# Kernel optimization log

Hardware: AMD Instinct MI355X
Metric: run time of the kernel (lower is better)

The kernel has to match this reference:

```python
import jax, jax.numpy as jnp
import numpy as np

N_USERS = 100000
N_ITEMS = 50000
N_EDGES = 1600000
EMBED = 128
LAYER = 128


def setup_inputs() -> dict:
    key = jax.random.key(0)
    k1, k2, k3, k4, k5 = jax.random.split(key, 5)
    item_emb = jax.random.normal(k1, (N_ITEMS, EMBED), dtype=jnp.float32)
    # per-user mean normalization (1/degree); use uniform positive values
    user_n_j = jax.random.uniform(k2, (N_USERS, 1), dtype=jnp.float32)
    mean_weight = jax.random.normal(k3, (EMBED, LAYER), dtype=jnp.float32) * (1.0 / np.sqrt(EMBED))
    adj_vals = jnp.ones((N_EDGES,), dtype=jnp.float32)
    adj_rows = jax.random.randint(k4, (N_EDGES,), 0, N_USERS, dtype=jnp.int32)
    adj_cols = jax.random.randint(k5, (N_EDGES,), 0, N_ITEMS, dtype=jnp.int32)
    return {
        "item_emb": item_emb,
        "user_n_j": user_n_j,
        "mean_weight": mean_weight,
        "adj_vals": adj_vals,
        "adj_rows": adj_rows,
        "adj_cols": adj_cols,
        "n_users": N_USERS,
    }


def reference(item_emb, user_n_j, mean_weight, adj_vals, adj_rows, adj_cols, n_users):
    # e_k = sparse.mm(adj, item_emb): gather item rows per edge, scale by edge
    # value, scatter-add into destination user rows.
    edge_feat = adj_vals[:, None] * item_emb[adj_cols]          # [E, D]
    e_k = jax.ops.segment_sum(edge_feat, adj_rows, num_segments=n_users)  # [U, D]
    e_k = e_k * user_n_j                                        # neighbor-mean scale
    return e_k @ mean_weight                                    # [U, layer]
```

## Files before the change

### kernel.cpp

```cpp
#include <hip/hip_runtime.h>
#include <hip/hip_bf16.h>

#define D 128
#define BSHIFT 6
#define BUSERS (1 << BSHIFT)
#define NBLK 256
#define CHUNK 1280
#define MROWS 64

typedef __attribute__((ext_vector_type(8))) short bf16x8;
typedef __attribute__((ext_vector_type(4))) float f32x4;

__device__ __forceinline__ unsigned int bf16rn(float f) {
  unsigned int u = __float_as_uint(f);
  return (u + 0x7fffu + ((u >> 16) & 1u)) >> 16;
}

__device__ __forceinline__ void pw_tile(
    const float* __restrict__ emb, const float* __restrict__ W,
    unsigned short* __restrict__ Pb, int n_items, int tile,
    unsigned short* Wt ) {
  const int tid = threadIdx.x;
  const int m0 = tile * MROWS;

  for (int i = tid; i < 128 * 128; i += 256) {
    const int k = i >> 7, c = i & 127;
    const unsigned short v = (unsigned short)bf16rn(W[i]);
    const int boff = c * 256 + ((2 * k) ^ ((c & 7) << 4));
    *reinterpret_cast<unsigned short*>(reinterpret_cast<char*>(Wt) + boff) = v;
  }

  const int w = tid >> 6;
  const int lane = tid & 63;
  const int lr = lane & 15;
  const int lg = lane >> 4;

  bf16x8 a[4];
  const int gr = m0 + w * 16 + lr;
#pragma unroll
  for (int ks = 0; ks < 4; ++ks) {
    float4 f0 = {0.f, 0.f, 0.f, 0.f}, f1 = {0.f, 0.f, 0.f, 0.f};
    if (gr < n_items) {
      const float* p = emb + (size_t)gr * 128 + ks * 32 + lg * 8;
      f0 = *reinterpret_cast<const float4*>(p);
      f1 = *reinterpret_cast<const float4*>(p + 4);
    }
    bf16x8 av;
    av[0] = (short)bf16rn(f0.x); av[1] = (short)bf16rn(f0.y);
    av[2] = (short)bf16rn(f0.z); av[3] = (short)bf16rn(f0.w);
    av[4] = (short)bf16rn(f1.x); av[5] = (short)bf16rn(f1.y);
    av[6] = (short)bf16rn(f1.z); av[7] = (short)bf16rn(f1.w);
    a[ks] = av;
  }
  __syncthreads();

  f32x4 acc[8];
#pragma unroll
  for (int cs = 0; cs < 8; ++cs) acc[cs] = {0.f, 0.f, 0.f, 0.f};

#pragma unroll
  for (int cs = 0; cs < 8; ++cs) {
    const int c = cs * 16 + lr;
#pragma unroll
    for (int ks = 0; ks < 4; ++ks) {
      const int boff = c * 256 + (((ks * 64) + lg * 16) ^ ((lr & 7) << 4));
      const bf16x8 b = *reinterpret_cast<const bf16x8*>(
          reinterpret_cast<const char*>(Wt) + boff);
      acc[cs] = __builtin_amdgcn_mfma_f32_16x16x32_bf16(a[ks], b, acc[cs],
                                                        0, 0, 0);
    }
  }

#pragma unroll
  for (int cs = 0; cs < 8; ++cs) {
    const int c = cs * 16 + lr;
#pragma unroll
    for (int reg = 0; reg < 4; ++reg) {
      const int r = m0 + w * 16 + lg * 4 + reg;
      if (r < n_items)
        Pb[(size_t)r * 128 + c] = (unsigned short)bf16rn(acc[cs][reg]);
    }
  }
}

__global__ __launch_bounds__(256) void pw_hist_kernel(
    const float* __restrict__ emb, const float* __restrict__ W,
    unsigned short* __restrict__ Pb, int n_items, int npw1,
    const int* __restrict__ rows, int* __restrict__ bcount, int n_edges,
    int epb, int nbuck) {
  __shared__ __align__(16) char smem[32768];
  const int tid = threadIdx.x;

  if ((int)blockIdx.x < npw1) {
    pw_tile(emb, W, Pb, n_items, blockIdx.x, (unsigned short*)smem);
  } else {
    int* h = (int*)smem;
    const int hb = blockIdx.x - npw1;
    for (int b = tid; b < nbuck; b += 256) h[b] = 0;
    __syncthreads();
    const int e0 = hb * epb;
    const int e1 = (e0 + epb < n_edges) ? e0 + epb : n_edges;
    for (int e = e0 + tid; e < e1; e += 256)
      atomicAdd(&h[rows[e] >> BSHIFT], 1);
    __syncthreads();
    for (int b = tid; b < nbuck; b += 256)
      bcount[(size_t)b * NBLK + hb] = h[b];
  }
}

__global__ __launch_bounds__(1024) void blocksum_kernel(
    const int* __restrict__ in, int* __restrict__ partials, int n) {
  __shared__ int lds[1024];
  const int tid = threadIdx.x;
  const int i = blockIdx.x * 1024 + tid;
  lds[tid] = (i < n) ? in[i] : 0;
  __syncthreads();
  for (int s = 512; s > 0; s >>= 1) {
    if (tid < s) lds[tid] += lds[tid + s];
    __syncthreads();
  }
  if (tid == 0) partials[blockIdx.x] = lds[0];
}

__global__ __launch_bounds__(1024) void scanpart_kernel(
    const int* __restrict__ partials, int* __restrict__ blockoff, int nb) {
  __shared__ int lds[1024];
  const int tid = threadIdx.x;
  const int x = (tid < nb) ? partials[tid] : 0;
  lds[tid] = x;
  __syncthreads();
  for (int s = 1; s < 1024; s <<= 1) {
    const int y = (tid >= s) ? lds[tid - s] : 0;
    __syncthreads();
    lds[tid] += y;
    __syncthreads();
  }
  if (tid < nb) blockoff[tid] = lds[tid] - x;
}

__global__ __launch_bounds__(1024) void localscan_kernel(
    const int* __restrict__ in, const int* __restrict__ blockoff,
    int* __restrict__ base, int n) {
  __shared__ int lds[1024];
  const int tid = threadIdx.x;
  const int i = blockIdx.x * 1024 + tid;
  const int x = (i < n) ? in[i] : 0;
  lds[tid] = x;
  __syncthreads();
  for (int s = 1; s < 1024; s <<= 1) {
    const int y = (tid >= s) ? lds[tid - s] : 0;
    __syncthreads();
    lds[tid] += y;
    __syncthreads();
  }
  if (i < n) base[i] = blockoff[blockIdx.x] + lds[tid] - x;
}

__global__ __launch_bounds__(256) void scatter_pw_kernel(
    const int* __restrict__ rows, const int* __restrict__ cols,
    const float* __restrict__ vals, const int* __restrict__ base,
    int2* __restrict__ sedge, int n_edges, int epb, int nbuck,
    const float* __restrict__ emb, const float* __restrict__ W,
    unsigned short* __restrict__ Pb, int n_items, int npw1) {
  __shared__ __align__(16) char smem[32768];
  const int tid = threadIdx.x;

  if ((int)blockIdx.x >= NBLK) {
    pw_tile(emb, W, Pb, n_items, npw1 + (int)blockIdx.x - NBLK,
            (unsigned short*)smem);
    return;
  }
  int* cur = (int*)smem;
  for (int b = tid; b < nbuck; b += 256)
    cur[b] = base[(size_t)b * NBLK + blockIdx.x];
  __syncthreads();
  const int e0 = blockIdx.x * epb;
  const int e1 = (e0 + epb < n_edges) ? e0 + epb : n_edges;
  for (int e = e0 + tid; e < e1; e += 256) {
    const int r = rows[e];
    const int pos = atomicAdd(&cur[r >> BSHIFT], 1);
    sedge[pos] =
        make_int2(((r & (BUSERS - 1)) << 16) | cols[e], __float_as_int(vals[e]));
  }
}

__global__ __launch_bounds__(256) void bucket_gather_kernel(
    const uint4* __restrict__ Pb4,
    const int* __restrict__ base, const int2* __restrict__ sedge,
    const float* __restrict__ nj, float* __restrict__ out, int n_users,
    int n_edges, int nbuck) {
  __shared__ int2 eraw[CHUNK];
  __shared__ int2 esort[CHUNK];
  __shared__ int cnt[BUSERS];
  __shared__ int incl[BUSERS];

  const int tid = threadIdx.x;
  const int b = blockIdx.x;
  const int u0 = b << BSHIFT;
  const int qw = tid >> 4;
  const int l16 = tid & 15;

  const int beg = base[(size_t)b * NBLK];
  const int end = (b + 1 < nbuck) ? base[(size_t)(b + 1) * NBLK] : n_edges;

  float4 acc0[4], acc1[4];
#pragma unroll
  for (int k = 0; k < 4; ++k) {
    acc0[k] = {0.f, 0.f, 0.f, 0.f};
    acc1[k] = {0.f, 0.f, 0.f, 0.f};
  }

  for (int cbeg = beg; cbeg < end; cbeg += CHUNK) {
    const int cnum = (cbeg + CHUNK < end) ? CHUNK : (end - cbeg);
    if (tid < BUSERS) cnt[tid] = 0;
    __syncthreads();
    for (int i = tid; i < cnum; i += 256) {
      const int2 e = sedge[cbeg + i];
      eraw[i] = e;
      atomicAdd(&cnt[((unsigned int)e.x) >> 16], 1);
    }
    __syncthreads();
    if (tid < BUSERS) incl[tid] = cnt[tid];
    __syncthreads();
    for (int s = 1; s < BUSERS; s <<= 1) {
      int y = 0;
      if (tid < BUSERS && tid >= s) y = incl[tid - s];
      __syncthreads();
      if (tid < BUSERS) incl[tid] += y;
      __syncthreads();
    }
    if (tid < BUSERS) cnt[tid] = incl[tid] - cnt[tid];
    __syncthreads();
    for (int i = tid; i < cnum; i += 256) {
      const int2 e = eraw[i];
      const int pos = atomicAdd(&cnt[((unsigned int)e.x) >> 16], 1);
      esort[pos] = e;
    }
    __syncthreads();

    if (cnum > 0) {
#pragma unroll
      for (int k = 0; k < 4; ++k) {
        const int ul = qw * 4 + k;
        const int s = (ul == 0) ? 0 : incl[ul - 1];
        const int t = incl[ul];
        const int ub = ((qw >> 2) << 4) + k;
        int wlen = 0;
#pragma unroll
        for (int m = 0; m < 4; ++m) {
          const int u2 = ub + m * 4;
          const int s2 = (u2 == 0) ? 0 : incl[u2 - 1];
          const int l2 = incl[u2] - s2;
          wlen = (l2 > wlen) ? l2 : wlen;
        }
        for (int i = 0; i < wlen; i += 8) {
          int2 e[8];
          uint4 p[8];
          float vv[8];
#pragma unroll
          for (int q = 0; q < 8; ++q) {
            const int j = s + i + q;
            const bool ok = (j < t);
            e[q] = esort[ok ? j : 0];
            vv[q] = ok ? __int_as_float(e[q].y) : 0.f;
          }
#pragma unroll
          for (int q = 0; q < 8; ++q)
            p[q] = Pb4[(size_t)(e[q].x & 0xffff) * 16 + l16];
#pragma unroll
          for (int q = 0; q < 8; ++q) {
            const float v = vv[q];
            acc0[k].x += v * __uint_as_float(p[q].x << 16);
            acc0[k].y += v * __uint_as_float(p[q].x & 0xffff0000u);
            acc0[k].z += v * __uint_as_float(p[q].y << 16);
            acc0[k].w += v * __uint_as_float(p[q].y & 0xffff0000u);
            acc1[k].x += v * __uint_as_float(p[q].z << 16);
            acc1[k].y += v * __uint_as_float(p[q].z & 0xffff0000u);
            acc1[k].z += v * __uint_as_float(p[q].w << 16);
            acc1[k].w += v * __uint_as_float(p[q].w & 0xffff0000u);
          }
        }
      }
    }
    __syncthreads();
  }

#pragma unroll
  for (int k = 0; k < 4; ++k) {
    const int u = u0 + qw * 4 + k;
    if (u < n_users) {
      const float s = nj[u];
      float4 a0 = acc0[k], a1 = acc1[k];
      a0.x *= s; a0.y *= s; a0.z *= s; a0.w *= s;
      a1.x *= s; a1.y *= s; a1.z *= s; a1.w *= s;
      float* o = out + (size_t)u * D + l16 * 8;
      *reinterpret_cast<float4*>(o) = a0;
      *reinterpret_cast<float4*>(o + 4) = a1;
    }
  }
}

extern "C" void kernel_launch(void* const* d_in, const int* in_sizes, int n_in,
                              void* d_out, int out_size, void* d_ws,
                              size_t ws_size, hipStream_t stream) {
  const float* item_emb = (const float*)d_in[0];
  const float* user_nj  = (const float*)d_in[1];
  const float* weight   = (const float*)d_in[2];
  const float* adj_vals = (const float*)d_in[3];
  const int*   adj_rows = (const int*)d_in[4];
  const int*   adj_cols = (const int*)d_in[5];

  const int n_items = in_sizes[0] / D;
  const int n_users = in_sizes[1];
  const int n_edges = in_sizes[3];
  float* out = (float*)d_out;

  const int nbuck = (n_users + BUSERS - 1) >> BSHIFT;
  const int npw = (n_items + MROWS - 1) / MROWS;
  const int npw1 = (npw + 1) / 2;
  const int npw2 = npw - npw1;
  const int epb = (n_edges + NBLK - 1) / NBLK;
  const int n_scan = nbuck * NBLK;
  const int nb_scan = (n_scan + 1023) / 1024;

  auto align256 = [](size_t x) { return (x + 255) & ~(size_t)255; };
  char* ws = (char*)d_ws;
  size_t off = 0;
  unsigned short* Pb = (unsigned short*)(ws + off);
  off = align256(off + (size_t)n_items * D * 2);
  int* bcount = (int*)(ws + off);  off = align256(off + (size_t)n_scan * 4);
  int* base = (int*)(ws + off);    off = align256(off + (size_t)n_scan * 4);
  int2* sedge = (int2*)(ws + off); off = align256(off + (size_t)n_edges * 8);
  int* partials = (int*)(ws + off); off = align256(off + (size_t)nb_scan * 4);
  int* blockoff = (int*)(ws + off); off = align256(off + (size_t)nb_scan * 4);

  pw_hist_kernel<<<npw1 + NBLK, 256, 0, stream>>>(
      item_emb, weight, Pb, n_items, npw1, adj_rows, bcount, n_edges, epb,
      nbuck);

  blocksum_kernel<<<nb_scan, 1024, 0, stream>>>(bcount, partials, n_scan);
  scanpart_kernel<<<1, 1024, 0, stream>>>(partials, blockoff, nb_scan);
  localscan_kernel<<<nb_scan, 1024, 0, stream>>>(bcount, blockoff, base,
                                                 n_scan);

  scatter_pw_kernel<<<NBLK + npw2, 256, 0, stream>>>(
      adj_rows, adj_cols, adj_vals, base, sedge, n_edges, epb, nbuck,
      item_emb, weight, Pb, n_items, npw1);

  bucket_gather_kernel<<<nbuck, 256, 0, stream>>>(
      reinterpret_cast<const uint4*>(Pb), base, sedge, user_nj, out,
      n_users, n_edges, nbuck);
}
```

Measured before the change: 112.1 us.

## Accumulate gather in packed fp16 FMA and fold partial scan into blocksum

The projected item table is now stored as fp16 instead of bf16, and the gather kernel accumulates with packed fp16x2 FMAs instead of unpacking bf16 to fp32 and doing scalar FMAs. This cuts ALU work per edge. Separately, the single-block partial scan kernel is removed: the last blocksum block, found with an atomic counter reset by the hist kernel, does the partials scan, which saves one launch. Accumulating in fp16 loses precision and risks overflow for users with many edges.

```diff
diff --git a/kernel.cpp b/kernel.cpp
--- a/kernel.cpp
+++ b/kernel.cpp
@@ -10,15 +10,20 @@
 
 typedef __attribute__((ext_vector_type(8))) short bf16x8;
 typedef __attribute__((ext_vector_type(4))) float f32x4;
+typedef _Float16 f16x2 __attribute__((ext_vector_type(2)));
 
 __device__ __forceinline__ unsigned int bf16rn(float f) {
   unsigned int u = __float_as_uint(f);
   return (u + 0x7fffu + ((u >> 16) & 1u)) >> 16;
 }
+__device__ __forceinline__ unsigned short fp16rn(float f) {
+  _Float16 h = (_Float16)f;
+  return *reinterpret_cast<unsigned short*>(&h);
+}
 
 __device__ __forceinline__ void pw_tile(
     const float* __restrict__ emb, const float* __restrict__ W,
-    unsigned short* __restrict__ Pb, int n_items, int tile,
+    unsigned short* __restrict__ Ph, int n_items, int tile,
     unsigned short* Wt ) {
   const int tid = threadIdx.x;
   const int m0 = tile * MROWS;
@@ -78,22 +83,23 @@
     for (int reg = 0; reg < 4; ++reg) {
       const int r = m0 + w * 16 + lg * 4 + reg;
       if (r < n_items)
-        Pb[(size_t)r * 128 + c] = (unsigned short)bf16rn(acc[cs][reg]);
+        Ph[(size_t)r * 128 + c] = fp16rn(acc[cs][reg]);
     }
   }
 }
 
 __global__ __launch_bounds__(256) void pw_hist_kernel(
     const float* __restrict__ emb, const float* __restrict__ W,
-    unsigned short* __restrict__ Pb, int n_items, int npw1,
+    unsigned short* __restrict__ Ph, int n_items, int npw1,
     const int* __restrict__ rows, int* __restrict__ bcount, int n_edges,
-    int epb, int nbuck) {
+    int epb, int nbuck, int* __restrict__ done) {
   __shared__ __align__(16) char smem[32768];
   const int tid = threadIdx.x;
 
   if ((int)blockIdx.x < npw1) {
-    pw_tile(emb, W, Pb, n_items, blockIdx.x, (unsigned short*)smem);
+    pw_tile(emb, W, Ph, n_items, blockIdx.x, (unsigned short*)smem);
   } else {
+    if ((int)blockIdx.x == npw1 && tid == 0) *done = 0;
     int* h = (int*)smem;
     const int hb = blockIdx.x - npw1;
     for (int b = tid; b < nbuck; b += 256) h[b] = 0;
@@ -109,8 +115,10 @@
 }
 
 __global__ __launch_bounds__(1024) void blocksum_kernel(
-    const int* __restrict__ in, int* __restrict__ partials, int n) {
+    const int* __restrict__ in, int* __restrict__ partials,
+    int* __restrict__ blockoff, int* __restrict__ done, int n, int nb) {
   __shared__ int lds[1024];
+  __shared__ int is_last;
   const int tid = threadIdx.x;
   const int i = blockIdx.x * 1024 + tid;
   lds[tid] = (i < n) ? in[i] : 0;
@@ -120,22 +128,25 @@
     __syncthreads();
   }
   if (tid == 0) partials[blockIdx.x] = lds[0];
-}
-
-__global__ __launch_bounds__(1024) void scanpart_kernel(
-    const int* __restrict__ partials, int* __restrict__ blockoff, int nb) {
-  __shared__ int lds[1024];
-  const int tid = threadIdx.x;
-  const int x = (tid < nb) ? partials[tid] : 0;
-  lds[tid] = x;
-  __syncthreads();
-  for (int s = 1; s < 1024; s <<= 1) {
-    const int y = (tid >= s) ? lds[tid - s] : 0;
-    __syncthreads();
-    lds[tid] += y;
-    __syncthreads();
-  }
-  if (tid < nb) blockoff[tid] = lds[tid] - x;
+  __threadfence();
+  if (tid == 0) {
+    const int t = atomicAdd(done, 1);
+    is_last = (t == nb - 1);
+  }
+  __syncthreads();
+  if (is_last) {
+    __threadfence();
+    const int x = (tid < nb) ? partials[tid] : 0;
+    lds[tid] = x;
+    __syncthreads();
+    for (int s = 1; s < 1024; s <<= 1) {
+      const int y = (tid >= s) ? lds[tid - s] : 0;
+      __syncthreads();
+      lds[tid] += y;
+      __syncthreads();
+    }
+    if (tid < nb) blockoff[tid] = lds[tid] - x;
+  }
 }
 
 __global__ __launch_bounds__(1024) void localscan_kernel(
@@ -161,12 +172,12 @@
     const float* __restrict__ vals, const int* __restrict__ base,
     int2* __restrict__ sedge, int n_edges, int epb, int nbuck,
     const float* __restrict__ emb, const float* __restrict__ W,
-    unsigned short* __restrict__ Pb, int n_items, int npw1) {
+    unsigned short* __restrict__ Ph, int n_items, int npw1) {
   __shared__ __align__(16) char smem[32768];
   const int tid = threadIdx.x;
 
   if ((int)blockIdx.x >= NBLK) {
-    pw_tile(emb, W, Pb, n_items, npw1 + (int)blockIdx.x - NBLK,
+    pw_tile(emb, W, Ph, n_items, npw1 + (int)blockIdx.x - NBLK,
             (unsigned short*)smem);
     return;
   }
@@ -185,7 +196,7 @@
 }
 
 __global__ __launch_bounds__(256) void bucket_gather_kernel(
-    const uint4* __restrict__ Pb4,
+    const uint4* __restrict__ Ph4,
     const int* __restrict__ base, const int2* __restrict__ sedge,
     const float* __restrict__ nj, float* __restrict__ out, int n_users,
     int n_edges, int nbuck) {
@@ -203,12 +214,11 @@
   const int beg = base[(size_t)b * NBLK];
   const int end = (b + 1 < nbuck) ? base[(size_t)(b + 1) * NBLK] : n_edges;
 
-  float4 acc0[4], acc1[4];
-#pragma unroll
-  for (int k = 0; k < 4; ++k) {
-    acc0[k] = {0.f, 0.f, 0.f, 0.f};
-    acc1[k] = {0.f, 0.f, 0.f, 0.f};
-  }
+  f16x2 acc[4][4];
+#pragma unroll
+  for (int k = 0; k < 4; ++k)
+#pragma unroll
+    for (int m = 0; m < 4; ++m) acc[k][m] = (f16x2){(_Float16)0, (_Float16)0};
 
   for (int cbeg = beg; cbeg < end; cbeg += CHUNK) {
     const int cnum = (cbeg + CHUNK < end) ? CHUNK : (end - cbeg);
@@ -256,28 +266,28 @@
         for (int i = 0; i < wlen; i += 8) {
           int2 e[8];
           uint4 p[8];
-          float vv[8];
+          _Float16 hv[8];
 #pragma unroll
           for (int q = 0; q < 8; ++q) {
             const int j = s + i + q;
             const bool ok = (j < t);
             e[q] = esort[ok ? j : 0];
-            vv[q] = ok ? __int_as_float(e[q].y) : 0.f;
+            hv[q] = (_Float16)(ok ? __int_as_float(e[q].y) : 0.f);
           }
 #pragma unroll
           for (int q = 0; q < 8; ++q)
-            p[q] = Pb4[(size_t)(e[q].x & 0xffff) * 16 + l16];
+            p[q] = Ph4[(size_t)(e[q].x & 0xffff) * 16 + l16];
 #pragma unroll
           for (int q = 0; q < 8; ++q) {
-            const float v = vv[q];
-            acc0[k].x += v * __uint_as_float(p[q].x << 16);
-            acc0[k].y += v * __uint_as_float(p[q].x & 0xffff0000u);
-            acc0[k].z += v * __uint_as_float(p[q].y << 16);
-            acc0[k].w += v * __uint_as_float(p[q].y & 0xffff0000u);
-            acc1[k].x += v * __uint_as_float(p[q].z << 16);
-            acc1[k].y += v * __uint_as_float(p[q].z & 0xffff0000u);
-            acc1[k].z += v * __uint_as_float(p[q].w << 16);
-            acc1[k].w += v * __uint_as_float(p[q].w & 0xffff0000u);
+            const f16x2 vh = {hv[q], hv[q]};
+            acc[k][0] = __builtin_elementwise_fma(
+                vh, __builtin_bit_cast(f16x2, p[q].x), acc[k][0]);
+            acc[k][1] = __builtin_elementwise_fma(
+                vh, __builtin_bit_cast(f16x2, p[q].y), acc[k][1]);
+            acc[k][2] = __builtin_elementwise_fma(
+                vh, __builtin_bit_cast(f16x2, p[q].z), acc[k][2]);
+            acc[k][3] = __builtin_elementwise_fma(
+                vh, __builtin_bit_cast(f16x2, p[q].w), acc[k][3]);
           }
         }
       }
@@ -290,9 +300,11 @@
     const int u = u0 + qw * 4 + k;
     if (u < n_users) {
       const float s = nj[u];
-      float4 a0 = acc0[k], a1 = acc1[k];
-      a0.x *= s; a0.y *= s; a0.z *= s; a0.w *= s;
-      a1.x *= s; a1.y *= s; a1.z *= s; a1.w *= s;
+      float4 a0, a1;
+      a0.x = (float)acc[k][0][0] * s; a0.y = (float)acc[k][0][1] * s;
+      a0.z = (float)acc[k][1][0] * s; a0.w = (float)acc[k][1][1] * s;
+      a1.x = (float)acc[k][2][0] * s; a1.y = (float)acc[k][2][1] * s;
+      a1.z = (float)acc[k][3][0] * s; a1.w = (float)acc[k][3][1] * s;
       float* o = out + (size_t)u * D + l16 * 8;
       *reinterpret_cast<float4*>(o) = a0;
       *reinterpret_cast<float4*>(o + 4) = a1;
@@ -326,28 +338,29 @@
   auto align256 = [](size_t x) { return (x + 255) & ~(size_t)255; };
   char* ws = (char*)d_ws;
   size_t off = 0;
-  unsigned short* Pb = (unsigned short*)(ws + off);
+  unsigned short* Ph = (unsigned short*)(ws + off);
   off = align256(off + (size_t)n_items * D * 2);
   int* bcount = (int*)(ws + off);  off = align256(off + (size_t)n_scan * 4);
   int* base = (int*)(ws + off);    off = align256(off + (size_t)n_scan * 4);
   int2* sedge = (int2*)(ws + off); off = align256(off + (size_t)n_edges * 8);
   int* partials = (int*)(ws + off); off = align256(off + (size_t)nb_scan * 4);
   int* blockoff = (int*)(ws + off); off = align256(off + (size_t)nb_scan * 4);
+  int* done = (int*)(ws + off);     off = align256(off + 4);
 
   pw_hist_kernel<<<npw1 + NBLK, 256, 0, stream>>>(
-      item_emb, weight, Pb, n_items, npw1, adj_rows, bcount, n_edges, epb,
-      nbuck);
-
-  blocksum_kernel<<<nb_scan, 1024, 0, stream>>>(bcount, partials, n_scan);
-  scanpart_kernel<<<1, 1024, 0, stream>>>(partials, blockoff, nb_scan);
+      item_emb, weight, Ph, n_items, npw1, adj_rows, bcount, n_edges, epb,
+      nbuck, done);
+
+  blocksum_kernel<<<nb_scan, 1024, 0, stream>>>(bcount, partials, blockoff,
+                                                done, n_scan, nb_scan);
   localscan_kernel<<<nb_scan, 1024, 0, stream>>>(bcount, blockoff, base,
                                                  n_scan);
 
   scatter_pw_kernel<<<NBLK + npw2, 256, 0, stream>>>(
       adj_rows, adj_cols, adj_vals, base, sedge, n_edges, epb, nbuck,
-      item_emb, weight, Pb, n_items, npw1);
+      item_emb, weight, Ph, n_items, npw1);
 
   bucket_gather_kernel<<<nbuck, 256, 0, stream>>>(
-      reinterpret_cast<const uint4*>(Pb), base, sedge, user_nj, out,
+      reinterpret_cast<const uint4*>(Ph), base, sedge, user_nj, out,
       n_users, n_edges, nbuck);
 }
```

Measured after the change: 209.9 us. 87.2% more time.
